# Kernel optimization log

Hardware: AMD Instinct MI355X
Metric: run time of the kernel (lower is better)

The kernel has to match this reference:

```python
import jax, jax.numpy as jnp
import numpy as np

T, B, IN, OUT = 128, 32, 128, 128
N, M, R, H = 256, 64, 4, 256  # mem_slot, mem_size, read_heads, nn_output_size


def setup_inputs() -> dict:
    key = jax.random.key(0)
    ks = jax.random.split(key, 10)
    s = 0.05
    return {
        "xs": jax.random.normal(ks[0], (T, B, IN), jnp.float32),
        "mem0": jax.random.normal(ks[1], (B, N, M), jnp.float32) * s,
        "W_lstm": jax.random.normal(ks[2], (IN + M * R + H, 4 * H), jnp.float32) * s,
        "b_lstm": jnp.zeros((4 * H,), jnp.float32),
        "W_pre": jax.random.normal(ks[3], (H, OUT), jnp.float32) * s,
        "b_pre": jnp.zeros((OUT,), jnp.float32),
        "W_key": jax.random.normal(ks[4], (H, M), jnp.float32) * s,
        "W_beta": jax.random.normal(ks[5], (H, 1), jnp.float32) * s,
        "W_teach": jax.random.normal(ks[6], (H, M), jnp.float32) * s,
        "W_ro": jax.random.normal(ks[7], (M * R, OUT), jnp.float32) * s,
    }


def reference(xs, mem0, W_lstm, b_lstm, W_pre, b_pre, W_key, W_beta, W_teach, W_ro):
    eps = 1e-8

    def step(carry, x):
        mem, h, c, read_vecs, loss = carry
        # controller: LSTM cell over [x, flattened read vectors]
        inp = jnp.concatenate([x, read_vecs.reshape(B, M * R)], axis=-1)
        z = jnp.concatenate([inp, h], axis=-1) @ W_lstm + b_lstm
        i, f, g, o = jnp.split(z, 4, axis=-1)
        c = jax.nn.sigmoid(f) * c + jax.nn.sigmoid(i) * jnp.tanh(g)
        h = jax.nn.sigmoid(o) * jnp.tanh(c)
        pre_out = h @ W_pre + b_pre          # (B, OUT)
        k = h @ W_key                        # (B, M) content key
        beta = jax.nn.softplus(h @ W_beta)   # (B, 1) sharpness
        teacher = h @ W_teach                # (B, M) generated teacher vec
        # cosine similarity between each memory slot and the key
        num = jnp.einsum('bnm,bm->bn', mem, k)
        den = jnp.maximum(
            jnp.linalg.norm(mem, axis=-1) * jnp.linalg.norm(k, axis=-1, keepdims=True), eps)
        sim = num / den                      # (B, N)
        write_w = jax.nn.softmax(beta * sim, axis=-1)  # safe_softmax over slots
        # additive content write (outer product of write weights and key)
        mem = mem + write_w[:, :, None] * k[:, None, :]
        # supervision loss: match generated teacher to written content
        loss = loss + jnp.mean((k - teacher) ** 2)
        # read: write_w broadcast over R heads -> identical reads per head
        read = jnp.einsum('bn,bnm->bm', write_w, mem)  # (B, M)
        read_vecs = jnp.broadcast_to(read[:, :, None], (B, M, R))
        out = pre_out + read_vecs.reshape(B, M * R) @ W_ro
        return (mem, h, c, read_vecs, loss), out

    carry0 = (mem0,
              jnp.zeros((B, H), xs.dtype),
              jnp.zeros((B, H), xs.dtype),
              jnp.zeros((B, M, R), xs.dtype),
              jnp.zeros((), xs.dtype))
    (_, _, _, _, sup_loss), ys = jax.lax.scan(step, carry0, xs)
    return ys, sup_loss
```

## Files before the change

### kernel.cpp

```cpp
#include <hip/hip_runtime.h>

typedef unsigned short u16;
typedef unsigned int u32;
typedef unsigned long long u64;
typedef short short8 __attribute__((ext_vector_type(8)));
typedef float f32x4 __attribute__((ext_vector_type(4)));

__device__ __forceinline__ float b2f(u16 u) {
    unsigned x = ((unsigned)u) << 16;
    return __builtin_bit_cast(float, x);
}
__device__ __forceinline__ u16 f2b(float f) {
    unsigned u = __builtin_bit_cast(unsigned, f);
    u += 0x7FFFu + ((u >> 16) & 1u);
    return (u16)(u >> 16);
}
__device__ __forceinline__ float sigm(float x) { return 1.f / (1.f + __expf(-x)); }
__device__ __forceinline__ float tanh_(float x) { return 1.f - 2.f / (__expf(2.f * x) + 1.f); }

__device__ __forceinline__ u64 lda(const u64* p) {
    return __hip_atomic_load(p, __ATOMIC_RELAXED, __HIP_MEMORY_SCOPE_AGENT);
}
__device__ __forceinline__ void sta(u64* p, u64 v) {
    __hip_atomic_store(p, v, __ATOMIC_RELAXED, __HIP_MEMORY_SCOPE_AGENT);
}
__device__ __forceinline__ unsigned ld_flag(const unsigned* p) {
    return __hip_atomic_load(p, __ATOMIC_RELAXED, __HIP_MEMORY_SCOPE_AGENT);
}
__device__ __forceinline__ void st_flag(unsigned* p, unsigned v) {
    __hip_atomic_store(p, v, __ATOMIC_RELAXED, __HIP_MEMORY_SCOPE_AGENT);
}
__device__ __forceinline__ void ld16x4_issue(const void* p0, const void* p1, const void* p2,
                                             const void* p3, uint4& a, uint4& b, uint4& c, uint4& d) {
    asm volatile(
        "global_load_dwordx4 %0, %4, off sc0 sc1\n\t"
        "global_load_dwordx4 %1, %5, off sc0 sc1\n\t"
        "global_load_dwordx4 %2, %6, off sc0 sc1\n\t"
        "global_load_dwordx4 %3, %7, off sc0 sc1"
        : "=v"(a), "=v"(b), "=v"(c), "=v"(d)
        : "v"(p0), "v"(p1), "v"(p2), "v"(p3) : "memory");
}
__device__ __forceinline__ void wait_vm0() {
    asm volatile("s_waitcnt vmcnt(0)" ::: "memory");
}
__device__ __forceinline__ void st16(void* p, uint4 v) {
    u64 lo = ((u64)v.y << 32) | (u64)v.x;
    u64 hi = ((u64)v.w << 32) | (u64)v.z;
    __hip_atomic_store((u64*)p,     lo, __ATOMIC_RELAXED, __HIP_MEMORY_SCOPE_AGENT);
    __hip_atomic_store((u64*)p + 1, hi, __ATOMIC_RELAXED, __HIP_MEMORY_SCOPE_AGENT);
}

#define T_STEPS 128
#define BATCH   32
#define KHR     320
#define PADK    328
#define MEMPAD  68
#define WKPAD   264

#define WS_BAR      0
#define WS_LOSS     128
#define WS_FLAG     160
#define WS_RT       192
#define WS_HRG      16576
#define WS_ZSET     41088
#define WS_XSF      41216
#define WS_MEM0F    2138368
#define WS_WLF      4235520
#define WS_BLF      6856960
#define WS_WPREF    6861056
#define WS_BPREF    6992128
#define WS_WKEYF    6992640
#define WS_WBETAF   7058176
#define WS_WTEACHF  7059200
#define WS_WROF     7124736
#define WS_XW       7255808
#define WS_WREFF    24033024
#define WS_WKT      24295168
#define WS_WROEFF   24360704
#define WS_HS       24393472
#define WS_RS       28587776

#define HR_OFF   0
#define WF_OFF   20992
#define WK_OFF   41472
#define MEM_OFF  75264
#define Z_OFF    144896
#define C_OFF    149504
#define KV_OFF   151552
#define WW_OFF   151808
#define KP_OFF   152832
#define RP_OFF   153856
#define BR_OFF   154880
#define WR_OFF   154944
#define SC_OFF   155008
#define WB_OFF   155072
#define HST_OFF  156096
#define RST_OFF  156608
#define LDS_TOTAL 156736

__device__ __forceinline__ void gridbar(unsigned* flags, unsigned phase, int rank) {
    __syncthreads();
    if (threadIdx.x < 64) {
        if (threadIdx.x == 0) st_flag(flags + rank, phase);
        long guard = 0;
        for (;;) {
            unsigned v = ld_flag(flags + (threadIdx.x & 31));
            if (__ballot(v < phase) == 0ull) break;
            if (++guard > 1000000L) break;
        }
    }
    __syncthreads();
}

__global__ void dnc_probe(const u16* __restrict__ xs_u16, char* __restrict__ ws) {
    __shared__ int cnt;
    if (threadIdx.x == 0) cnt = 0;
    __syncthreads();
    int c = 0;
    for (int i = threadIdx.x; i < 1024; i += 256) {
        int e = (xs_u16[i] >> 7) & 0xFF;
        if (e >= 96 && e <= 135) c++;
    }
    atomicAdd(&cnt, c);
    __syncthreads();
    if (threadIdx.x == 0) *(int*)(ws + WS_FLAG) = (cnt > 820) ? 1 : 0;
}

__global__ void dnc_normalize(const void* s0, const void* s1, const void* s2, const void* s3,
                              const void* s4, const void* s5, const void* s6, const void* s7,
                              const void* s8, const void* s9, char* __restrict__ ws) {
    const void* srcs[10] = {s0, s1, s2, s3, s4, s5, s6, s7, s8, s9};
    const int sizes[10] = {524288, 524288, 655360, 1024, 32768, 128, 16384, 256, 16384, 32768};
    const int bases[10] = {WS_XSF, WS_MEM0F, WS_WLF, WS_BLF, WS_WPREF, WS_BPREF,
                           WS_WKEYF, WS_WBETAF, WS_WTEACHF, WS_WROF};
    const int bf = *(const int*)(ws + WS_FLAG);
    const int gt = blockIdx.x * 256 + threadIdx.x, gs = gridDim.x * 256;
    for (int s = 0; s < 10; ++s) {
        float* dst = (float*)(ws + bases[s]);
        const int n = sizes[s];
        if (bf) {
            const u16* p = (const u16*)srcs[s];
            for (int i = gt; i < n; i += gs) dst[i] = b2f(p[i]);
        } else {
            const float* p = (const float*)srcs[s];
            for (int i = gt; i < n; i += gs) dst[i] = p[i];
        }
    }
}

__global__ void dnc_prologue(char* __restrict__ ws) {
    extern __shared__ float xls[];
    const float* XSF     = (const float*)(ws + WS_XSF);
    const float* WLF     = (const float*)(ws + WS_WLF);
    const float* BLF     = (const float*)(ws + WS_BLF);
    const float* WKEYF   = (const float*)(ws + WS_WKEYF);
    const float* WTEACHF = (const float*)(ws + WS_WTEACHF);
    const float* WROF    = (const float*)(ws + WS_WROF);
    float* xW  = (float*)(ws + WS_XW);
    float* WrE = (float*)(ws + WS_WREFF);
    float* Wkt = (float*)(ws + WS_WKT);
    float* Wre = (float*)(ws + WS_WROEFF);
    const int wg = blockIdx.x, tid = threadIdx.x;
    if (wg < 256) {
        const int rb = wg >> 3, cb = wg & 7;
        const float4* xsrc = (const float4*)(XSF + (size_t)rb * 16384);
        for (int i = tid; i < 4096; i += 256) {
            float4 v = xsrc[i];
            int row = i >> 5, c4 = (i & 31) * 4;
            float* d = xls + row * 129 + c4;
            d[0] = v.x; d[1] = v.y; d[2] = v.z; d[3] = v.w;
        }
        __syncthreads();
        const int tr = tid >> 4, tc = tid & 15;
        const int c0 = cb * 128 + tc * 8;
        float acc[8][8];
#pragma unroll
        for (int rr = 0; rr < 8; ++rr)
#pragma unroll
            for (int cc = 0; cc < 8; ++cc) acc[rr][cc] = BLF[c0 + cc];
        for (int k = 0; k < 128; ++k) {
            float4 wA = *(const float4*)(WLF + (size_t)k * 1024 + c0);
            float4 wB = *(const float4*)(WLF + (size_t)k * 1024 + c0 + 4);
            float w[8] = {wA.x, wA.y, wA.z, wA.w, wB.x, wB.y, wB.z, wB.w};
#pragma unroll
            for (int rr = 0; rr < 8; ++rr) {
                float xv = xls[(tr * 8 + rr) * 129 + k];
#pragma unroll
                for (int cc = 0; cc < 8; ++cc) acc[rr][cc] += xv * w[cc];
            }
        }
#pragma unroll
        for (int rr = 0; rr < 8; ++rr) {
            size_t o = (size_t)(rb * 128 + tr * 8 + rr) * 1024 + c0;
            *(float4*)(xW + o)     = make_float4(acc[rr][0], acc[rr][1], acc[rr][2], acc[rr][3]);
            *(float4*)(xW + o + 4) = make_float4(acc[rr][4], acc[rr][5], acc[rr][6], acc[rr][7]);
        }
    } else if (wg < 320) {
        const int m = wg - 256;
        const int c = tid * 4;
#pragma unroll
        for (int e = 0; e < 4; ++e) {
            float s = 0.f;
#pragma unroll
            for (int rr = 0; rr < 4; ++rr) s += WLF[(size_t)(128 + 4 * m + rr) * 1024 + c + e];
            WrE[m * 1024 + c + e] = s;
        }
    } else if (wg < 336) {
        const int i = (wg - 320) * 1024 + tid * 4;
#pragma unroll
        for (int e = 0; e < 4; ++e) Wkt[i + e] = WKEYF[i + e] - WTEACHF[i + e];
    } else if (wg < 344) {
        const int i = (wg - 336) * 1024 + tid * 4;
#pragma unroll
        for (int e = 0; e < 4; ++e) {
            int m = (i + e) >> 7, c = (i + e) & 127;
            float s = 0.f;
#pragma unroll
            for (int rr = 0; rr < 4; ++rr) s += WROF[(4 * m + rr) * 128 + c];
            Wre[i + e] = s;
        }
    }
}

__global__ __launch_bounds__(256, 1) void dnc_main(char* __restrict__ ws) {
    extern __shared__ char smem[];
    u16*   hr_lds = (u16*)(smem + HR_OFF);
    u16*   wfrag  = (u16*)(smem + WF_OFF);
    u16*   wkeyT  = (u16*)(smem + WK_OFF);
    float* memA   = (float*)(smem + MEM_OFF);
    float* z_lds  = (float*)(smem + Z_OFF);
    float* c_lds  = (float*)(smem + C_OFF);
    float* kv     = (float*)(smem + KV_OFF);
    float* wwts   = (float*)(smem + WW_OFF);
    float* kpart  = (float*)(smem + KP_OFF);
    float* rp     = (float*)(smem + RP_OFF);
    float* bred   = (float*)(smem + BR_OFF);
    float* wred   = (float*)(smem + WR_OFF);
    float* sc     = (float*)(smem + SC_OFF);
    float* wbF    = (float*)(smem + WB_OFF);
    u16*   hstage = (u16*)(smem + HST_OFF);
    u16*   rstage = (u16*)(smem + RST_OFF);

    const int tid  = threadIdx.x;
    const int wg   = blockIdx.x;
    const int lane = tid & 63;
    const int wid  = tid >> 6;

    unsigned* flags = (unsigned*)(ws + WS_BAR);
    u64* rT         = (u64*)(ws + WS_RT);
    u16* hrg        = (u16*)(ws + WS_HRG);
    const float* xWF     = (const float*)(ws + WS_XW);
    const float* WrEffF  = (const float*)(ws + WS_WREFF);
    const float* WLF     = (const float*)(ws + WS_WLF);
    const float* WKEYF   = (const float*)(ws + WS_WKEYF);
    const float* WBETAF  = (const float*)(ws + WS_WBETAF);
    const float* MEM0F   = (const float*)(ws + WS_MEM0F);
    float* HsF = (float*)(ws + WS_HS);
    float* RsF = (float*)(ws + WS_RS);

    for (int i = tid; i < 32 * PADK; i += 256) hr_lds[i] = 0;
    for (int idx = tid; idx < 10240; idx += 256) {
        int k = idx >> 5, c = idx & 31;
        int kt = k >> 5, q = (k >> 3) & 3, j = k & 7;
        int gcol = (c >> 3) * 256 + wg * 8 + (c & 7);
        float v = (k < 64) ? WrEffF[k * 1024 + gcol]
                           : WLF[(size_t)(384 + (k - 64)) * 1024 + gcol];
        wfrag[((kt * 4 + q) * 32 + c) * 8 + j] = f2b(v);
    }
    for (int i = tid; i < 256 * 64; i += 256) {
        int k = i >> 6, m = i & 63;
        wkeyT[m * WKPAD + k] = f2b(WKEYF[i]);
    }
    wbF[tid]   = WBETAF[tid];
    c_lds[tid] = 0.f;
    for (int i = tid; i < 256 * 64; i += 256) {
        int n = i >> 6, m = i & 63;
        memA[n * MEMPAD + m] = MEM0F[wg * 16384 + i];
    }
    __syncthreads();

    const int bt = wid & 1, ct = wid >> 1;
    const int fm = lane & 15, fq = lane >> 4;
    const int pb = tid >> 3, pu = tid & 7;

    float xg0, xg1, xg2, xg3;
    {
        const size_t xb = (size_t)pb * 1024 + wg * 8 + pu;
        xg0 = xWF[xb]; xg1 = xWF[xb + 256]; xg2 = xWF[xb + 512]; xg3 = xWF[xb + 768];
    }
    f32x4 hWacc = {0.f, 0.f, 0.f, 0.f};

    for (int t = 0; t < T_STEPS; ++t) {
        {
            const u64* rch = rT + (size_t)((((t + 1) & 1) * 32 + pb) * 16 + 2 * pu) * 2;
            const u32 want = (u32)t;
            u64 v0, v1, v2, v3;
            long guard = 0;
            for (;;) {
                v0 = lda(rch); v1 = lda(rch + 1); v2 = lda(rch + 2); v3 = lda(rch + 3);
                bool ok = ((u32)v0 == want) && ((u32)(v1 >> 32) == want) &&
                          ((u32)v2 == want) && ((u32)(v3 >> 32) == want);
                if (ok) break;
                if (++guard > 200000L) break;
            }
            u32* dst = (u32*)hr_lds + pb * 164 + 4 * pu;
            dst[0] = (u32)(v0 >> 32); dst[1] = (u32)v1;
            dst[2] = (u32)(v2 >> 32); dst[3] = (u32)v3;
        }
        __syncthreads();

        f32x4 acc = hWacc;
#pragma unroll
        for (int kt = 0; kt < 2; ++kt) {
            short8 a = *(const short8*)(hr_lds + (bt * 16 + fm) * PADK + kt * 32 + fq * 8);
            short8 b = *(const short8*)(wfrag + ((kt * 4 + fq) * 32 + ct * 16 + fm) * 8);
            acc = __builtin_amdgcn_mfma_f32_16x16x32_bf16(a, b, acc, 0, 0, 0);
        }
#pragma unroll
        for (int r = 0; r < 4; ++r) {
            int bb = bt * 16 + fq * 4 + r;
            int cc = ct * 16 + fm;
            z_lds[bb * 36 + cc] = acc[r];
        }
        __syncthreads();

        {
            float iv = z_lds[pb * 36 + pu]      + xg0;
            float fv = z_lds[pb * 36 + 8 + pu]  + xg1;
            float gv = z_lds[pb * 36 + 16 + pu] + xg2;
            float ov = z_lds[pb * 36 + 24 + pu] + xg3;
            float co = c_lds[pb * 8 + pu];
            float cn = sigm(fv) * co + sigm(iv) * tanh_(gv);
            float hn = sigm(ov) * tanh_(cn);
            c_lds[pb * 8 + pu] = cn;
            hstage[pb * 8 + pu] = f2b(hn);
            HsF[(size_t)(t * BATCH + pb) * 256 + wg * 8 + pu] = hn;
        }
        __syncthreads();
        if (tid < 32) {
            uint4 hv = *(const uint4*)(hstage + tid * 8);
            st16(hrg + tid * KHR + 64 + wg * 8, hv);
        }
        gridbar(flags, (unsigned)(t + 1), wg);

        uint4 ha, hb4, hc, hd;
        {
            const u16* src = hrg + pb * KHR + 64 + pu * 32;
            ld16x4_issue(src, src + 8, src + 16, src + 24, ha, hb4, hc, hd);
        }
        {
            int tn = (t + 1 < T_STEPS) ? t + 1 : 127;
            const size_t xb = (size_t)(tn * BATCH + pb) * 1024 + wg * 8 + pu;
            xg0 = xWF[xb]; xg1 = xWF[xb + 256]; xg2 = xWF[xb + 512]; xg3 = xWF[xb + 768];
        }
        float nr2 = 0.f;
        {
            const float4* mrow = (const float4*)(memA + tid * MEMPAD);
#pragma unroll
            for (int i = 0; i < 16; ++i) {
                float4 m4 = mrow[i];
                nr2 += m4.x * m4.x + m4.y * m4.y + m4.z * m4.z + m4.w * m4.w;
            }
        }
        wait_vm0();
        {
            u16* dst = hr_lds + pb * PADK + 64 + pu * 32;
            *(uint4*)(dst)      = ha;
            *(uint4*)(dst + 8)  = hb4;
            *(uint4*)(dst + 16) = hc;
            *(uint4*)(dst + 24) = hd;
        }
        __syncthreads();

        {
            f32x4 hz = {0.f, 0.f, 0.f, 0.f};
#pragma unroll
            for (int kt = 2; kt < 10; ++kt) {
                short8 a = *(const short8*)(hr_lds + (bt * 16 + fm) * PADK + kt * 32 + fq * 8);
                short8 b = *(const short8*)(wfrag + ((kt * 4 + fq) * 32 + ct * 16 + fm) * 8);
                hz = __builtin_amdgcn_mfma_f32_16x16x32_bf16(a, b, hz, 0, 0, 0);
            }
            hWacc = hz;
        }

        const u16* hrow = hr_lds + wg * PADK + 64;
        {
            float a = 0.f;
#pragma unroll
            for (int i = 0; i < 8; ++i) {
                short8 w8 = *(const short8*)(wkeyT + lane * WKPAD + wid * 64 + i * 8);
                short8 h8 = *(const short8*)(hrow + wid * 64 + i * 8);
#pragma unroll
                for (int e = 0; e < 8; ++e)
                    a += b2f((u16)h8[e]) * b2f((u16)w8[e]);
            }
            kpart[wid * 64 + lane] = a;
        }
        {
            float bp = b2f(hrow[tid]) * wbF[tid];
#pragma unroll
            for (int off = 32; off > 0; off >>= 1) bp += __shfl_xor(bp, off, 64);
            if (lane == 0) bred[wid] = bp;
        }
        __syncthreads();
        if (tid < 64) {
            float kk = kpart[tid] + kpart[64 + tid] + kpart[128 + tid] + kpart[192 + tid];
            kv[tid] = kk;
            float k2 = kk * kk;
#pragma unroll
            for (int off = 32; off > 0; off >>= 1) k2 += __shfl_xor(k2, off, 64);
            if (tid == 0) sc[1] = sqrtf(k2);
        } else if (tid == 64) {
            float zb = bred[0] + bred[1] + bred[2] + bred[3];
            sc[0] = logf(1.f + __expf(zb));
        }
        __syncthreads();
        const float beta = sc[0], knorm = sc[1];

        float num = 0.f;
        {
            const float4* mrow = (const float4*)(memA + tid * MEMPAD);
            const float4* k4p  = (const float4*)kv;
#pragma unroll
            for (int i = 0; i < 16; ++i) {
                float4 m4 = mrow[i], k4 = k4p[i];
                num += m4.x * k4.x + m4.y * k4.y + m4.z * k4.z + m4.w * k4.w;
            }
        }
        float den = fmaxf(sqrtf(nr2) * knorm, 1e-8f);
        float s   = beta * (num / den);
        float wm = s;
#pragma unroll
        for (int off = 32; off > 0; off >>= 1) wm = fmaxf(wm, __shfl_xor(wm, off, 64));
        float ev = __expf(s - wm);
        float wsum = ev;
#pragma unroll
        for (int off = 32; off > 0; off >>= 1) wsum += __shfl_xor(wsum, off, 64);
        if (lane == 0) { wred[wid] = wm; wred[8 + wid] = wsum; }
        __syncthreads();
        float gm = fmaxf(fmaxf(wred[0], wred[1]), fmaxf(wred[2], wred[3]));
        float gsum = wred[8]  * __expf(wred[0] - gm) + wred[9]  * __expf(wred[1] - gm)
                   + wred[10] * __expf(wred[2] - gm) + wred[11] * __expf(wred[3] - gm);
        float w = __expf(s - gm) / gsum;
        wwts[tid] = w;
        {
            float w2 = w * w;
#pragma unroll
            for (int off = 32; off > 0; off >>= 1) w2 += __shfl_xor(w2, off, 64);
            if (lane == 0) bred[wid] = w2;
        }
        __syncthreads();
        const float wsq = bred[0] + bred[1] + bred[2] + bred[3];

        {
            const int lm = lane & 15, q = lane >> 4;
            float r0 = 0.f, r1 = 0.f, r2 = 0.f, r3 = 0.f;
#pragma unroll
            for (int i = 0; i < 16; ++i) {
                int n = wid * 64 + i * 4 + q;
                float wn = wwts[n];
                float4 m4 = *(const float4*)(memA + n * MEMPAD + 4 * lm);
                r0 += wn * m4.x; r1 += wn * m4.y; r2 += wn * m4.z; r3 += wn * m4.w;
            }
            r0 += __shfl_xor(r0, 16, 64); r0 += __shfl_xor(r0, 32, 64);
            r1 += __shfl_xor(r1, 16, 64); r1 += __shfl_xor(r1, 32, 64);
            r2 += __shfl_xor(r2, 16, 64); r2 += __shfl_xor(r2, 32, 64);
            r3 += __shfl_xor(r3, 16, 64); r3 += __shfl_xor(r3, 32, 64);
            if (q == 0) {
                rp[wid * 64 + 4 * lm + 0] = r0;
                rp[wid * 64 + 4 * lm + 1] = r1;
                rp[wid * 64 + 4 * lm + 2] = r2;
                rp[wid * 64 + 4 * lm + 3] = r3;
            }
        }
        __syncthreads();
        if (tid < 64) {
            float rd = rp[tid] + rp[64 + tid] + rp[128 + tid] + rp[192 + tid]
                     + wsq * kv[tid];
            rstage[tid] = f2b(rd);
            RsF[(size_t)(t * BATCH + wg) * 64 + tid] = rd;
        }
        __syncthreads();
        if (tid < 16) {
            const u32* rs32 = (const u32*)rstage;
            u32 w0 = rs32[2 * tid], w1 = rs32[2 * tid + 1];
            u64* dstc = rT + (size_t)(((t & 1) * 32 + wg) * 16 + tid) * 2;
            const u64 tag = (u64)(u32)(t + 1);
            sta(dstc,     ((u64)w0 << 32) | tag);
            sta(dstc + 1, (tag << 32) | w1);
        }
        {
            const int lm = lane & 15, q = lane >> 4;
            float4 k4 = ((const float4*)kv)[lm];
#pragma unroll
            for (int i = 0; i < 16; ++i) {
                int n = wid * 64 + i * 4 + q;
                float wn = wwts[n];
                float4* mp = (float4*)(memA + n * MEMPAD + 4 * lm);
                float4 m4 = *mp;
                m4.x += wn * k4.x; m4.y += wn * k4.y; m4.z += wn * k4.z; m4.w += wn * k4.w;
                *mp = m4;
            }
        }
    }
}

__global__ void dnc_epilogue(char* __restrict__ ws, void* __restrict__ outv) {
    __shared__ float hs8[8][256];
    __shared__ float rs8[8][64];
    __shared__ float lacc;
    const float* HsF   = (const float*)(ws + WS_HS);
    const float* RsF   = (const float*)(ws + WS_RS);
    const float* WktF  = (const float*)(ws + WS_WKT);
    const float* WreF  = (const float*)(ws + WS_WROEFF);
    const float* WpreF = (const float*)(ws + WS_WPREF);
    const float* bpreF = (const float*)(ws + WS_BPREF);
    float* lossacc = (float*)(ws + WS_LOSS);
    const int bf = *(const int*)(ws + WS_FLAG);
    const int tid = threadIdx.x;
    const size_t r0 = (size_t)blockIdx.x * 8;
    if (tid == 0) lacc = 0.f;
    for (int i = tid; i < 8 * 256; i += 256) hs8[i >> 8][i & 255] = HsF[r0 * 256 + i];
    for (int i = tid; i < 8 * 64; i += 256)  rs8[i >> 6][i & 63]  = RsF[r0 * 64 + i];
    __syncthreads();
    {
        const int rl = tid >> 5, c0 = (tid & 31) * 4;
        float a0 = bpreF[c0], a1 = bpreF[c0 + 1], a2 = bpreF[c0 + 2], a3 = bpreF[c0 + 3];
        for (int k = 0; k < 256; ++k) {
            float hv = hs8[rl][k];
            float4 w4 = *(const float4*)(WpreF + k * 128 + c0);
            a0 += hv * w4.x; a1 += hv * w4.y; a2 += hv * w4.z; a3 += hv * w4.w;
        }
        for (int m = 0; m < 64; ++m) {
            float rv = rs8[rl][m];
            float4 w4 = *(const float4*)(WreF + m * 128 + c0);
            a0 += rv * w4.x; a1 += rv * w4.y; a2 += rv * w4.z; a3 += rv * w4.w;
        }
        size_t o = (r0 + rl) * 128 + c0;
        if (bf) {
            u16* out = (u16*)outv;
            out[o] = f2b(a0); out[o + 1] = f2b(a1); out[o + 2] = f2b(a2); out[o + 3] = f2b(a3);
        } else {
            float* out = (float*)outv;
            out[o] = a0; out[o + 1] = a1; out[o + 2] = a2; out[o + 3] = a3;
        }
    }
    {
        const int rl = tid >> 5, m0 = (tid & 31) * 2;
        float d0 = 0.f, d1 = 0.f;
        for (int k = 0; k < 256; ++k) {
            float hv = hs8[rl][k];
            d0 += hv * WktF[k * 64 + m0];
            d1 += hv * WktF[k * 64 + m0 + 1];
        }
        float p = d0 * d0 + d1 * d1;
#pragma unroll
        for (int off = 32; off > 0; off >>= 1) p += __shfl_xor(p, off, 64);
        if ((tid & 63) == 0) atomicAdd(&lacc, p);
        __syncthreads();
        if (tid == 0) atomicAdd(lossacc, lacc);
    }
}

__global__ void dnc_loss_fin(const char* __restrict__ ws, void* __restrict__ outv) {
    if (threadIdx.x == 0 && blockIdx.x == 0) {
        float l = *(const float*)(ws + WS_LOSS) * (1.f / 2048.f);
        if (*(const int*)(ws + WS_FLAG)) ((u16*)outv)[524288] = f2b(l);
        else                             ((float*)outv)[524288] = l;
    }
}

extern "C" void kernel_launch(void* const* d_in, const int* in_sizes, int n_in,
                              void* d_out, int out_size, void* d_ws, size_t ws_size,
                              hipStream_t stream) {
    char* ws = (char*)d_ws;
    hipMemsetAsync(d_ws, 0, WS_ZSET, stream);
    dnc_probe<<<1, 256, 0, stream>>>((const u16*)d_in[0], ws);
    dnc_normalize<<<512, 256, 0, stream>>>(d_in[0], d_in[1], d_in[2], d_in[3], d_in[4],
                                           d_in[5], d_in[6], d_in[7], d_in[8], d_in[9], ws);
    (void)hipFuncSetAttribute((const void*)dnc_prologue,
                              hipFuncAttributeMaxDynamicSharedMemorySize, 128 * 129 * 4);
    dnc_prologue<<<344, 256, 128 * 129 * 4, stream>>>(ws);
    (void)hipFuncSetAttribute((const void*)dnc_main,
                              hipFuncAttributeMaxDynamicSharedMemorySize, LDS_TOTAL);
    dnc_main<<<32, 256, LDS_TOTAL, stream>>>(ws);
    dnc_epilogue<<<512, 256, 0, stream>>>(ws, d_out);
    dnc_loss_fin<<<1, 64, 0, stream>>>(ws, d_out);
}
```

Measured before the change: 1.076 ms.

## Fuse probe into normalize, split prologue GEMM finer, streamline softmax reductions

Several independent changes land together. The dtype probe kernel is merged into the normalize kernel, so every block recomputes the flag and one launch disappears. The prologue x·W GEMM tile is halved to 8x4 per thread across 512 blocks for more parallelism. In the main recurrent kernel, the sum of squared write weights is computed alongside the softmax denominator, which removes one block barrier and the LDS write-weight buffer; weights are fetched by wave shuffle instead. Spin-waits gain s_sleep backoff and a larger guard, which may add wake-up latency on the critical per-step barrier.

Result: faster. 1.040 ms (-3.3%).

```diff
diff --git a/kernel.cpp b/kernel.cpp
--- a/kernel.cpp
+++ b/kernel.cpp
@@ -87,7 +87,6 @@
 #define Z_OFF    144896
 #define C_OFF    149504
 #define KV_OFF   151552
-#define WW_OFF   151808
 #define KP_OFF   152832
 #define RP_OFF   153856
 #define BR_OFF   154880
@@ -107,33 +106,34 @@
             unsigned v = ld_flag(flags + (threadIdx.x & 31));
             if (__ballot(v < phase) == 0ull) break;
             if (++guard > 1000000L) break;
+            if (guard > 4) __builtin_amdgcn_s_sleep(1);
         }
     }
     __syncthreads();
 }
 
-__global__ void dnc_probe(const u16* __restrict__ xs_u16, char* __restrict__ ws) {
+__global__ void dnc_normalize(const void* s0, const void* s1, const void* s2, const void* s3,
+                              const void* s4, const void* s5, const void* s6, const void* s7,
+                              const void* s8, const void* s9, char* __restrict__ ws) {
     __shared__ int cnt;
     if (threadIdx.x == 0) cnt = 0;
     __syncthreads();
-    int c = 0;
-    for (int i = threadIdx.x; i < 1024; i += 256) {
-        int e = (xs_u16[i] >> 7) & 0xFF;
-        if (e >= 96 && e <= 135) c++;
-    }
-    atomicAdd(&cnt, c);
+    {
+        const u16* xs_u16 = (const u16*)s0;
+        int c = 0;
+        for (int i = threadIdx.x; i < 1024; i += 256) {
+            int e = (xs_u16[i] >> 7) & 0xFF;
+            if (e >= 96 && e <= 135) c++;
+        }
+        atomicAdd(&cnt, c);
+    }
     __syncthreads();
-    if (threadIdx.x == 0) *(int*)(ws + WS_FLAG) = (cnt > 820) ? 1 : 0;
-}
-
-__global__ void dnc_normalize(const void* s0, const void* s1, const void* s2, const void* s3,
-                              const void* s4, const void* s5, const void* s6, const void* s7,
-                              const void* s8, const void* s9, char* __restrict__ ws) {
+    const int bf = (cnt > 820) ? 1 : 0;
+    if (blockIdx.x == 0 && threadIdx.x == 0) *(int*)(ws + WS_FLAG) = bf;
     const void* srcs[10] = {s0, s1, s2, s3, s4, s5, s6, s7, s8, s9};
     const int sizes[10] = {524288, 524288, 655360, 1024, 32768, 128, 16384, 256, 16384, 32768};
     const int bases[10] = {WS_XSF, WS_MEM0F, WS_WLF, WS_BLF, WS_WPREF, WS_BPREF,
                            WS_WKEYF, WS_WBETAF, WS_WTEACHF, WS_WROF};
-    const int bf = *(const int*)(ws + WS_FLAG);
     const int gt = blockIdx.x * 256 + threadIdx.x, gs = gridDim.x * 256;
     for (int s = 0; s < 10; ++s) {
         float* dst = (float*)(ws + bases[s]);
@@ -161,8 +161,8 @@
     float* Wkt = (float*)(ws + WS_WKT);
     float* Wre = (float*)(ws + WS_WROEFF);
     const int wg = blockIdx.x, tid = threadIdx.x;
-    if (wg < 256) {
-        const int rb = wg >> 3, cb = wg & 7;
+    if (wg < 512) {
+        const int rb = wg >> 4, cb = wg & 15;
         const float4* xsrc = (const float4*)(XSF + (size_t)rb * 16384);
         for (int i = tid; i < 4096; i += 256) {
             float4 v = xsrc[i];
@@ -172,31 +172,29 @@
         }
         __syncthreads();
         const int tr = tid >> 4, tc = tid & 15;
-        const int c0 = cb * 128 + tc * 8;
-        float acc[8][8];
-#pragma unroll
-        for (int rr = 0; rr < 8; ++rr)
-#pragma unroll
-            for (int cc = 0; cc < 8; ++cc) acc[rr][cc] = BLF[c0 + cc];
+        const int c0 = cb * 64 + tc * 4;
+        float acc[8][4];
+#pragma unroll
+        for (int rr = 0; rr < 8; ++rr) {
+            acc[rr][0] = BLF[c0]; acc[rr][1] = BLF[c0 + 1];
+            acc[rr][2] = BLF[c0 + 2]; acc[rr][3] = BLF[c0 + 3];
+        }
         for (int k = 0; k < 128; ++k) {
-            float4 wA = *(const float4*)(WLF + (size_t)k * 1024 + c0);
-            float4 wB = *(const float4*)(WLF + (size_t)k * 1024 + c0 + 4);
-            float w[8] = {wA.x, wA.y, wA.z, wA.w, wB.x, wB.y, wB.z, wB.w};
+            float4 w4 = *(const float4*)(WLF + (size_t)k * 1024 + c0);
 #pragma unroll
             for (int rr = 0; rr < 8; ++rr) {
                 float xv = xls[(tr * 8 + rr) * 129 + k];
-#pragma unroll
-                for (int cc = 0; cc < 8; ++cc) acc[rr][cc] += xv * w[cc];
+                acc[rr][0] += xv * w4.x; acc[rr][1] += xv * w4.y;
+                acc[rr][2] += xv * w4.z; acc[rr][3] += xv * w4.w;
             }
         }
 #pragma unroll
         for (int rr = 0; rr < 8; ++rr) {
             size_t o = (size_t)(rb * 128 + tr * 8 + rr) * 1024 + c0;
-            *(float4*)(xW + o)     = make_float4(acc[rr][0], acc[rr][1], acc[rr][2], acc[rr][3]);
-            *(float4*)(xW + o + 4) = make_float4(acc[rr][4], acc[rr][5], acc[rr][6], acc[rr][7]);
-        }
-    } else if (wg < 320) {
-        const int m = wg - 256;
+            *(float4*)(xW + o) = make_float4(acc[rr][0], acc[rr][1], acc[rr][2], acc[rr][3]);
+        }
+    } else if (wg < 576) {
+        const int m = wg - 512;
         const int c = tid * 4;
 #pragma unroll
         for (int e = 0; e < 4; ++e) {
@@ -205,12 +203,12 @@
             for (int rr = 0; rr < 4; ++rr) s += WLF[(size_t)(128 + 4 * m + rr) * 1024 + c + e];
             WrE[m * 1024 + c + e] = s;
         }
-    } else if (wg < 336) {
-        const int i = (wg - 320) * 1024 + tid * 4;
+    } else if (wg < 592) {
+        const int i = (wg - 576) * 1024 + tid * 4;
 #pragma unroll
         for (int e = 0; e < 4; ++e) Wkt[i + e] = WKEYF[i + e] - WTEACHF[i + e];
-    } else if (wg < 344) {
-        const int i = (wg - 336) * 1024 + tid * 4;
+    } else if (wg < 600) {
+        const int i = (wg - 592) * 1024 + tid * 4;
 #pragma unroll
         for (int e = 0; e < 4; ++e) {
             int m = (i + e) >> 7, c = (i + e) & 127;
@@ -231,7 +229,6 @@
     float* z_lds  = (float*)(smem + Z_OFF);
     float* c_lds  = (float*)(smem + C_OFF);
     float* kv     = (float*)(smem + KV_OFF);
-    float* wwts   = (float*)(smem + WW_OFF);
     float* kpart  = (float*)(smem + KP_OFF);
     float* rp     = (float*)(smem + RP_OFF);
     float* bred   = (float*)(smem + BR_OFF);
@@ -301,7 +298,8 @@
                 bool ok = ((u32)v0 == want) && ((u32)(v1 >> 32) == want) &&
                           ((u32)v2 == want) && ((u32)(v3 >> 32) == want);
                 if (ok) break;
-                if (++guard > 200000L) break;
+                if (++guard > 2000000L) break;
+                if (guard > 4) __builtin_amdgcn_s_sleep(1);
             }
             u32* dst = (u32*)hr_lds + pb * 164 + 4 * pu;
             dst[0] = (u32)(v0 >> 32); dst[1] = (u32)v1;
@@ -433,33 +431,30 @@
 #pragma unroll
         for (int off = 32; off > 0; off >>= 1) wm = fmaxf(wm, __shfl_xor(wm, off, 64));
         float ev = __expf(s - wm);
-        float wsum = ev;
-#pragma unroll
-        for (int off = 32; off > 0; off >>= 1) wsum += __shfl_xor(wsum, off, 64);
-        if (lane == 0) { wred[wid] = wm; wred[8 + wid] = wsum; }
+        float wsum = ev, wsumsq = ev * ev;
+#pragma unroll
+        for (int off = 32; off > 0; off >>= 1) {
+            wsum   += __shfl_xor(wsum, off, 64);
+            wsumsq += __shfl_xor(wsumsq, off, 64);
+        }
+        if (lane == 0) { wred[wid] = wm; wred[4 + wid] = wsum; wred[8 + wid] = wsumsq; }
         __syncthreads();
         float gm = fmaxf(fmaxf(wred[0], wred[1]), fmaxf(wred[2], wred[3]));
-        float gsum = wred[8]  * __expf(wred[0] - gm) + wred[9]  * __expf(wred[1] - gm)
-                   + wred[10] * __expf(wred[2] - gm) + wred[11] * __expf(wred[3] - gm);
-        float w = __expf(s - gm) / gsum;
-        wwts[tid] = w;
-        {
-            float w2 = w * w;
-#pragma unroll
-            for (int off = 32; off > 0; off >>= 1) w2 += __shfl_xor(w2, off, 64);
-            if (lane == 0) bred[wid] = w2;
-        }
-        __syncthreads();
-        const float wsq = bred[0] + bred[1] + bred[2] + bred[3];
+        float e0 = __expf(wred[0] - gm), e1 = __expf(wred[1] - gm);
+        float e2 = __expf(wred[2] - gm), e3 = __expf(wred[3] - gm);
+        float gsum  = wred[4] * e0 + wred[5] * e1 + wred[6] * e2 + wred[7] * e3;
+        float gsumq = wred[8] * e0 * e0 + wred[9] * e1 * e1
+                    + wred[10] * e2 * e2 + wred[11] * e3 * e3;
+        float w   = __expf(s - gm) / gsum;
+        float wsq = gsumq / (gsum * gsum);
 
         {
             const int lm = lane & 15, q = lane >> 4;
             float r0 = 0.f, r1 = 0.f, r2 = 0.f, r3 = 0.f;
 #pragma unroll
             for (int i = 0; i < 16; ++i) {
-                int n = wid * 64 + i * 4 + q;
-                float wn = wwts[n];
-                float4 m4 = *(const float4*)(memA + n * MEMPAD + 4 * lm);
+                float wn = __shfl(w, i * 4 + q, 64);
+                float4 m4 = *(const float4*)(memA + (wid * 64 + i * 4 + q) * MEMPAD + 4 * lm);
                 r0 += wn * m4.x; r1 += wn * m4.y; r2 += wn * m4.z; r3 += wn * m4.w;
             }
             r0 += __shfl_xor(r0, 16, 64); r0 += __shfl_xor(r0, 32, 64);
@@ -494,9 +489,8 @@
             float4 k4 = ((const float4*)kv)[lm];
 #pragma unroll
             for (int i = 0; i < 16; ++i) {
-                int n = wid * 64 + i * 4 + q;
-                float wn = wwts[n];
-                float4* mp = (float4*)(memA + n * MEMPAD + 4 * lm);
+                float wn = __shfl(w, i * 4 + q, 64);
+                float4* mp = (float4*)(memA + (wid * 64 + i * 4 + q) * MEMPAD + 4 * lm);
                 float4 m4 = *mp;
                 m4.x += wn * k4.x; m4.y += wn * k4.y; m4.z += wn * k4.z; m4.w += wn * k4.w;
                 *mp = m4;
@@ -575,12 +569,11 @@
                               hipStream_t stream) {
     char* ws = (char*)d_ws;
     hipMemsetAsync(d_ws, 0, WS_ZSET, stream);
-    dnc_probe<<<1, 256, 0, stream>>>((const u16*)d_in[0], ws);
     dnc_normalize<<<512, 256, 0, stream>>>(d_in[0], d_in[1], d_in[2], d_in[3], d_in[4],
                                            d_in[5], d_in[6], d_in[7], d_in[8], d_in[9], ws);
     (void)hipFuncSetAttribute((const void*)dnc_prologue,
                               hipFuncAttributeMaxDynamicSharedMemorySize, 128 * 129 * 4);
-    dnc_prologue<<<344, 256, 128 * 129 * 4, stream>>>(ws);
+    dnc_prologue<<<600, 256, 128 * 129 * 4, stream>>>(ws);
     (void)hipFuncSetAttribute((const void*)dnc_main,
                               hipFuncAttributeMaxDynamicSharedMemorySize, LDS_TOTAL);
     dnc_main<<<32, 256, LDS_TOTAL, stream>>>(ws);
```
